# Optimization experiments

Hardware: AMD Instinct MI355X
Metric: run time of the kernel (lower is better)

## Reference

```python
import math
import jax, jax.numpy as jnp
import numpy as np

B, T, D, H, HD, FF = 2, 2048, 768, 12, 64, 3072


def setup_inputs() -> dict:
    key = jax.random.key(0)
    ks = jax.random.split(key, 9)
    s = 0.02  # init scale
    x = jax.random.normal(ks[0], (B, T, D), jnp.float32)
    wq = jax.random.normal(ks[1], (D, D), jnp.float32) * s
    wk = jax.random.normal(ks[2], (D, D), jnp.float32) * s
    wv = jax.random.normal(ks[3], (D, D), jnp.float32) * s
    wo = jax.random.normal(ks[4], (D, D), jnp.float32) * s
    w1 = jax.random.normal(ks[5], (FF, D), jnp.float32) * s
    w2 = jax.random.normal(ks[6], (FF, D), jnp.float32) * s
    w3 = jax.random.normal(ks[7], (D, FF), jnp.float32) * s
    attn_norm_w = jnp.ones((D,), jnp.float32)
    ffn_norm_w = jnp.ones((D,), jnp.float32)
    # interleaved RoPE cache: values pair-repeated along head_dim
    inv_freq = 1.0 / (10000.0 ** (np.arange(0, HD, 2, dtype=np.float32) / HD))
    freqs = np.arange(T, dtype=np.float32)[:, None] * inv_freq[None, :]  # [T, HD/2]
    emb = np.repeat(freqs, 2, axis=-1)  # [T, HD]
    cos = jnp.asarray(np.cos(emb), jnp.float32)[None, None]  # [1,1,T,HD]
    sin = jnp.asarray(np.sin(emb), jnp.float32)[None, None]
    return {"x": x, "wq": wq, "wk": wk, "wv": wv, "wo": wo,
            "w1": w1, "w2": w2, "w3": w3,
            "attn_norm_w": attn_norm_w, "ffn_norm_w": ffn_norm_w,
            "cos": cos, "sin": sin}


def _rmsnorm(x, w, eps=1e-6):
    n = jnp.linalg.norm(x, axis=-1, keepdims=True)
    return w * x / (n / math.sqrt(x.shape[-1]) + eps)


def _rotate_half(x):
    x1, x2 = x[..., ::2], x[..., 1::2]
    return jnp.stack((-x2, x1), axis=-1).reshape(x.shape)


def _attention(x, wq, wk, wv, wo, cos, sin):
    b, t, c = x.shape
    q = (x @ wq.T).reshape(b, t, H, HD).transpose(0, 2, 1, 3)  # [B,H,T,hd]
    k = (x @ wk.T).reshape(b, t, H, HD).transpose(0, 2, 1, 3)
    v = (x @ wv.T).reshape(b, t, H, HD).transpose(0, 2, 1, 3)
    c_, s_ = cos[:, :, :t, :], sin[:, :, :t, :]
    q = q * c_ + _rotate_half(q) * s_
    k = k * c_ + _rotate_half(k) * s_
    att = jnp.einsum('bhqd,bhkd->bhqk', q, k) / math.sqrt(HD)
    mask = jnp.triu(jnp.full((t, t), -jnp.inf, att.dtype), k=1)
    att = jax.nn.softmax(att + mask, axis=-1)
    y = jnp.einsum('bhqk,bhkd->bhqd', att, v)
    y = y.transpose(0, 2, 1, 3).reshape(b, t, c)
    return y @ wo.T


def reference(x, wq, wk, wv, wo, w1, w2, w3, attn_norm_w, ffn_norm_w, cos, sin):
    x = x + _attention(_rmsnorm(x, attn_norm_w), wq, wk, wv, wo, cos, sin)
    h = _rmsnorm(x, ffn_norm_w)
    ff = (jax.nn.silu(h @ w1.T) * (h @ w2.T)) @ w3.T
    return x + ff
```

## Files before the change

kernel.cpp:

```cpp
#include <hip/hip_runtime.h>
#include <hip/hip_bf16.h>
#include <math.h>

typedef __bf16 bf16;
typedef __bf16 bf16x4 __attribute__((ext_vector_type(4)));
typedef __bf16 bf16x8 __attribute__((ext_vector_type(8)));
typedef float floatx4 __attribute__((ext_vector_type(4)));

#define T_ 2048
#define D_ 768
#define H_ 12
#define HD_ 64
#define FF_ 3072
#define LOG2E 1.44269504f
#define LDP 72

__device__ __forceinline__ floatx4 mfma_bf16(bf16x8 a, bf16x8 b, floatx4 c) {
  return __builtin_amdgcn_mfma_f32_16x16x32_bf16(a, b, c, 0, 0, 0);
}

__global__ __launch_bounds__(256)
void cvt_k(const float* __restrict__ wq, const float* __restrict__ wk,
           const float* __restrict__ wv, const float* __restrict__ wo,
           const float* __restrict__ w1, const float* __restrict__ w2,
           const float* __restrict__ w3, bf16* __restrict__ o) {
  const long i = ((long)blockIdx.x * 256 + threadIdx.x) * 8;
  const float* s;
  if      (i <  589824) s = wq + i;
  else if (i < 1179648) s = wk + (i -  589824);
  else if (i < 1769472) s = wv + (i - 1179648);
  else if (i < 2359296) s = wo + (i - 1769472);
  else if (i < 4718592) s = w1 + (i - 2359296);
  else if (i < 7077888) s = w2 + (i - 4718592);
  else                  s = w3 + (i - 7077888);
  const floatx4 a = *(const floatx4*)s;
  const floatx4 b = *(const floatx4*)(s + 4);
  bf16x8 r;
#pragma unroll
  for (int j = 0; j < 4; j++) { r[j] = (bf16)a[j]; r[4 + j] = (bf16)b[j]; }
  *(bf16x8*)&o[i] = r;
}

__device__ __forceinline__ void gemm128_core(
    const bf16* __restrict__ A, const bf16* __restrict__ W,
    bf16* __restrict__ C, int N, int K, int m0, int n0)
{
  __shared__ __align__(16) bf16 As[128 * LDP];
  __shared__ __align__(16) bf16 Ws[128 * LDP];

  const int tid = threadIdx.x;
  const int lane = tid & 63;
  const int wm = tid >> 7;
  const int wn = (tid >> 6) & 1;
  const int fr = lane & 15;
  const int fk = (lane >> 4) * 8;

  floatx4 acc[4][4] = {};

  const int ar = tid >> 3;
  const int ac = (tid & 7) * 8;
  const bf16* Aptr = A + (long)(m0 + ar) * K + ac;
  const bf16* Wptr = W + (long)(n0 + ar) * K + ac;
  const long rstep = (long)32 * K;

  bf16x8 apf[4], wpf[4];
#pragma unroll
  for (int c = 0; c < 4; c++) apf[c] = *(const bf16x8*)(Aptr + c * rstep);
#pragma unroll
  for (int c = 0; c < 4; c++) wpf[c] = *(const bf16x8*)(Wptr + c * rstep);

  const int ns = K >> 6;
  for (int ks = 0; ks < ns; ks++) {
    __syncthreads();
#pragma unroll
    for (int c = 0; c < 4; c++) *(bf16x8*)&As[(ar + c * 32) * LDP + ac] = apf[c];
#pragma unroll
    for (int c = 0; c < 4; c++) *(bf16x8*)&Ws[(ar + c * 32) * LDP + ac] = wpf[c];
    __syncthreads();
    const long koff = (long)((ks + 1 < ns) ? ks + 1 : ks) * 64;
#pragma unroll
    for (int c = 0; c < 4; c++) apf[c] = *(const bf16x8*)(Aptr + koff + c * rstep);
#pragma unroll
    for (int c = 0; c < 4; c++) wpf[c] = *(const bf16x8*)(Wptr + koff + c * rstep);
#pragma unroll
    for (int kc = 0; kc < 2; kc++) {
      bf16x8 af[4], bfv[4];
#pragma unroll
      for (int i = 0; i < 4; i++) af[i]  = *(const bf16x8*)&As[(wm * 64 + i * 16 + fr) * LDP + kc * 32 + fk];
#pragma unroll
      for (int j = 0; j < 4; j++) bfv[j] = *(const bf16x8*)&Ws[(wn * 64 + j * 16 + fr) * LDP + kc * 32 + fk];
#pragma unroll
      for (int i = 0; i < 4; i++)
#pragma unroll
        for (int j = 0; j < 4; j++)
          acc[i][j] = mfma_bf16(af[i], bfv[j], acc[i][j]);
    }
  }

  const int rb = (lane >> 4) * 4;
#pragma unroll
  for (int i = 0; i < 4; i++)
#pragma unroll
    for (int j = 0; j < 4; j++) {
      const int n = n0 + wn * 64 + j * 16 + fr;
#pragma unroll
      for (int r = 0; r < 4; r++) {
        const int m = m0 + wm * 64 + i * 16 + rb + r;
        C[(long)m * N + n] = (bf16)acc[i][j][r];
      }
    }
}

__global__ __launch_bounds__(256)
void gemm_qkv(const bf16* __restrict__ h, const bf16* __restrict__ wq,
              const bf16* __restrict__ wk, const bf16* __restrict__ wv,
              bf16* __restrict__ q, bf16* __restrict__ k, bf16* __restrict__ v) {
  const int widx = blockIdx.x / 6;
  const int nb   = blockIdx.x % 6;
  const bf16* W = (widx == 0) ? wq : (widx == 1) ? wk : wv;
  bf16*       O = (widx == 0) ? q  : (widx == 1) ? k  : v;
  gemm128_core(h, W, O, D_, D_, blockIdx.y * 128, nb * 128);
}

__global__ __launch_bounds__(256)
void gemm_n64(const bf16* __restrict__ A, const bf16* __restrict__ W,
              float* __restrict__ C, const float* __restrict__ resid,
              int N, int K) {
  __shared__ __align__(16) bf16 As[128 * LDP];
  __shared__ __align__(16) bf16 Ws[64 * LDP];

  const int L  = blockIdx.x;
  const int j  = L >> 3;
  const int mb = (L & 7) * 4 + (j / 12);
  const int nb = j % 12;
  const int m0 = mb * 128, n0 = nb * 64;

  const int tid = threadIdx.x;
  const int lane = tid & 63;
  const int wm = tid >> 7;
  const int wn = (tid >> 6) & 1;
  const int fr = lane & 15;
  const int fk = (lane >> 4) * 8;

  floatx4 acc[4][2] = {};

  const int ar = tid >> 3;
  const int ac = (tid & 7) * 8;
  const bf16* Aptr = A + (long)(m0 + ar) * K + ac;
  const bf16* Wptr = W + (long)(n0 + ar) * K + ac;
  const long rstep = (long)32 * K;

  bf16x8 apf[4], wpf[2];
#pragma unroll
  for (int c = 0; c < 4; c++) apf[c] = *(const bf16x8*)(Aptr + c * rstep);
#pragma unroll
  for (int c = 0; c < 2; c++) wpf[c] = *(const bf16x8*)(Wptr + c * rstep);

  const int ns = K >> 6;
  for (int ks = 0; ks < ns; ks++) {
    __syncthreads();
#pragma unroll
    for (int c = 0; c < 4; c++) *(bf16x8*)&As[(ar + c * 32) * LDP + ac] = apf[c];
#pragma unroll
    for (int c = 0; c < 2; c++) *(bf16x8*)&Ws[(ar + c * 32) * LDP + ac] = wpf[c];
    __syncthreads();
    const long koff = (long)((ks + 1 < ns) ? ks + 1 : ks) * 64;
#pragma unroll
    for (int c = 0; c < 4; c++) apf[c] = *(const bf16x8*)(Aptr + koff + c * rstep);
#pragma unroll
    for (int c = 0; c < 2; c++) wpf[c] = *(const bf16x8*)(Wptr + koff + c * rstep);
#pragma unroll
    for (int kc = 0; kc < 2; kc++) {
      bf16x8 af[4], bfv[2];
#pragma unroll
      for (int i = 0; i < 4; i++) af[i]  = *(const bf16x8*)&As[(wm * 64 + i * 16 + fr) * LDP + kc * 32 + fk];
#pragma unroll
      for (int j2 = 0; j2 < 2; j2++) bfv[j2] = *(const bf16x8*)&Ws[(wn * 32 + j2 * 16 + fr) * LDP + kc * 32 + fk];
#pragma unroll
      for (int i = 0; i < 4; i++)
#pragma unroll
        for (int j2 = 0; j2 < 2; j2++)
          acc[i][j2] = mfma_bf16(af[i], bfv[j2], acc[i][j2]);
    }
  }

  const int rb = (lane >> 4) * 4;
#pragma unroll
  for (int i = 0; i < 4; i++)
#pragma unroll
    for (int j2 = 0; j2 < 2; j2++) {
      const int n = n0 + wn * 32 + j2 * 16 + fr;
#pragma unroll
      for (int r = 0; r < 4; r++) {
        const int m = m0 + wm * 64 + i * 16 + rb + r;
        const long idx = (long)m * N + n;
        C[idx] = acc[i][j2][r] + resid[idx];
      }
    }
}

__global__ __launch_bounds__(256)
void gemm_w12(const bf16* __restrict__ A, const bf16* __restrict__ W1,
              const bf16* __restrict__ W2, bf16* __restrict__ G) {
  __shared__ __align__(16) bf16 As[128 * LDP];
  __shared__ __align__(16) bf16 W1s[64 * LDP];
  __shared__ __align__(16) bf16 W2s[64 * LDP];

  const int L  = blockIdx.x;
  const int j  = L >> 3;
  const int nb = (L & 7) * 6 + (j >> 5);
  const int mb = j & 31;
  const int m0 = mb * 128, n0 = nb * 64;
  const int K = D_;

  const int tid = threadIdx.x;
  const int lane = tid & 63;
  const int wm = tid >> 7;
  const int wn = (tid >> 6) & 1;
  const int fr = lane & 15;
  const int fk = (lane >> 4) * 8;

  floatx4 acc1[4][2] = {}, acc2[4][2] = {};

  const int ar = tid >> 3;
  const int ac = (tid & 7) * 8;
  const bf16* Aptr  = A  + (long)(m0 + ar) * K + ac;
  const bf16* W1ptr = W1 + (long)(n0 + ar) * K + ac;
  const bf16* W2ptr = W2 + (long)(n0 + ar) * K + ac;
  const long rstep = (long)32 * K;

  bf16x8 apf[4], w1pf[2], w2pf[2];
#pragma unroll
  for (int c = 0; c < 4; c++) apf[c] = *(const bf16x8*)(Aptr + c * rstep);
#pragma unroll
  for (int c = 0; c < 2; c++) { w1pf[c] = *(const bf16x8*)(W1ptr + c * rstep);
                                w2pf[c] = *(const bf16x8*)(W2ptr + c * rstep); }

  const int ns = K >> 6;
  for (int ks = 0; ks < ns; ks++) {
    __syncthreads();
#pragma unroll
    for (int c = 0; c < 4; c++) *(bf16x8*)&As[(ar + c * 32) * LDP + ac] = apf[c];
#pragma unroll
    for (int c = 0; c < 2; c++) { *(bf16x8*)&W1s[(ar + c * 32) * LDP + ac] = w1pf[c];
                                  *(bf16x8*)&W2s[(ar + c * 32) * LDP + ac] = w2pf[c]; }
    __syncthreads();
    const long koff = (long)((ks + 1 < ns) ? ks + 1 : ks) * 64;
#pragma unroll
    for (int c = 0; c < 4; c++) apf[c] = *(const bf16x8*)(Aptr + koff + c * rstep);
#pragma unroll
    for (int c = 0; c < 2; c++) { w1pf[c] = *(const bf16x8*)(W1ptr + koff + c * rstep);
                                  w2pf[c] = *(const bf16x8*)(W2ptr + koff + c * rstep); }
#pragma unroll
    for (int kc = 0; kc < 2; kc++) {
      bf16x8 af[4], b1[2], b2[2];
#pragma unroll
      for (int i = 0; i < 4; i++) af[i] = *(const bf16x8*)&As[(wm * 64 + i * 16 + fr) * LDP + kc * 32 + fk];
#pragma unroll
      for (int j2 = 0; j2 < 2; j2++) { b1[j2] = *(const bf16x8*)&W1s[(wn * 32 + j2 * 16 + fr) * LDP + kc * 32 + fk];
                                       b2[j2] = *(const bf16x8*)&W2s[(wn * 32 + j2 * 16 + fr) * LDP + kc * 32 + fk]; }
#pragma unroll
      for (int i = 0; i < 4; i++)
#pragma unroll
        for (int j2 = 0; j2 < 2; j2++) {
          acc1[i][j2] = mfma_bf16(af[i], b1[j2], acc1[i][j2]);
          acc2[i][j2] = mfma_bf16(af[i], b2[j2], acc2[i][j2]);
        }
    }
  }

  const int rb = (lane >> 4) * 4;
#pragma unroll
  for (int i = 0; i < 4; i++)
#pragma unroll
    for (int j2 = 0; j2 < 2; j2++) {
      const int n = n0 + wn * 32 + j2 * 16 + fr;
#pragma unroll
      for (int r = 0; r < 4; r++) {
        const int m = m0 + wm * 64 + i * 16 + rb + r;
        const float a1 = acc1[i][j2][r];
        const float a2 = acc2[i][j2][r];
        const float s = a1 / (1.f + exp2f(-a1 * LOG2E));
        G[(long)m * FF_ + n] = (bf16)(s * a2);
      }
    }
}

__global__ __launch_bounds__(256)
void rmsnorm_k(const float* __restrict__ x, const float* __restrict__ wt,
               bf16* __restrict__ o) {
  const int row = blockIdx.x;
  const int tid = threadIdx.x;
  const long off = (long)row * D_;
  float vals[3];
  float ss = 0.f;
#pragma unroll
  for (int i = 0; i < 3; i++) {
    vals[i] = x[off + tid + i * 256];
    ss += vals[i] * vals[i];
  }
#pragma unroll
  for (int d = 1; d < 64; d <<= 1) ss += __shfl_xor(ss, d);
  __shared__ float wsum[4];
  if ((tid & 63) == 0) wsum[tid >> 6] = ss;
  __syncthreads();
  const float tot = wsum[0] + wsum[1] + wsum[2] + wsum[3];
  const float inv = 1.0f / (sqrtf(tot * (1.0f / 768.0f)) + 1e-6f);
#pragma unroll
  for (int i = 0; i < 3; i++)
    o[off + tid + i * 256] = (bf16)(vals[i] * inv * wt[tid + i * 256]);
}

__global__ __launch_bounds__(256)
void rope_k(bf16* __restrict__ q, bf16* __restrict__ k,
            const float* __restrict__ cosb, const float* __restrict__ sinb) {
  const int idx = blockIdx.x * 256 + threadIdx.x;
  const int tkn = idx / 384;
  const int p   = idx % 384;
  const int hh  = p >> 5;
  const int i   = p & 31;
  const int pos = tkn & (T_ - 1);
  const long off = (long)tkn * D_ + hh * HD_ + 2 * i;
  const float c0 = cosb[pos * HD_ + 2 * i];
  const float c1 = cosb[pos * HD_ + 2 * i + 1];
  const float s0 = sinb[pos * HD_ + 2 * i];
  const float s1 = sinb[pos * HD_ + 2 * i + 1];
  const float qe = (float)q[off], qo = (float)q[off + 1];
  q[off]     = (bf16)(qe * c0 - qo * s0);
  q[off + 1] = (bf16)(qo * c1 + qe * s1);
  const float ke = (float)k[off], ko = (float)k[off + 1];
  k[off]     = (bf16)(ke * c0 - ko * s0);
  k[off + 1] = (bf16)(ko * c1 + ke * s1);
}

__global__ __launch_bounds__(256)
void vtrans_k(const bf16* __restrict__ v, bf16* __restrict__ vt) {
  const int bh = blockIdx.x >> 5;
  const int tt = blockIdx.x & 31;
  const int b = bh / H_, h = bh % H_;
  __shared__ __align__(16) bf16 Vs[64][72];
  const int tid = threadIdx.x;
  const int row = tid >> 2;
  const int c0  = (tid & 3) * 16;
  const long gin = ((long)(b * T_ + tt * 64 + row)) * D_ + h * HD_ + c0;
  *(bf16x8*)&Vs[row][c0]     = *(const bf16x8*)&v[gin];
  *(bf16x8*)&Vs[row][c0 + 8] = *(const bf16x8*)&v[gin + 8];
  __syncthreads();
  const int hd = tid >> 2;
  const int t0 = (tid & 3) * 16;
  bf16x8 o0, o1;
#pragma unroll
  for (int j = 0; j < 8; j++) { o0[j] = Vs[t0 + j][hd]; o1[j] = Vs[t0 + 8 + j][hd]; }
  const long gout = ((long)(bh * HD_ + hd)) * T_ + tt * 64 + t0;
  *(bf16x8*)&vt[gout]     = o0;
  *(bf16x8*)&vt[gout + 8] = o1;
}

__global__ __launch_bounds__(256, 4)
void flash_attn(const bf16* __restrict__ q, const bf16* __restrict__ k,
                const bf16* __restrict__ vtg, float* __restrict__ po,
                float* __restrict__ pm, float* __restrict__ pl) {
  const int gid = blockIdx.x;
  const int bh = gid / 80;
  const int r  = gid % 80;
  int qt, c;
  if (r < 8)       { qt = r; c = 0; }
  else if (r < 24) { qt = 8 + ((r - 8) >> 1); c = (r - 8) & 1; }
  else if (r < 48) { const int u = r - 24; const int d = u / 3; qt = 16 + d; c = u - d * 3; }
  else             { const int u = r - 48; qt = 24 + (u >> 2); c = u & 3; }
  const int b  = bh / H_;
  const int h  = bh % H_;
  const int q0 = qt * 64;
  const int tbeg = c * 8;
  const int tend = (tbeg + 7 < qt) ? tbeg + 7 : qt;

  __shared__ __align__(16) bf16 Qs[64][72];
  __shared__ __align__(16) bf16 Ks[64][72];
  __shared__ __align__(16) bf16 Vt[64][72];
  __shared__ __align__(16) bf16 Ps[4][16][72];

  const int tid = threadIdx.x, lane = tid & 63, w = tid >> 6;
  const int fr = lane & 15, quad = lane >> 4, fk = quad * 8;
  const long base = ((long)b * T_) * D_ + h * HD_;
  const long vbase = (long)bh * HD_ * T_;

  {
    const int srow = tid >> 2, scol = (tid & 3) * 16;
    const long g = base + (long)(q0 + srow) * D_ + scol;
    *(bf16x8*)&Qs[srow][scol]     = *(const bf16x8*)&q[g];
    *(bf16x8*)&Qs[srow][scol + 8] = *(const bf16x8*)&q[g + 8];
  }

  float m_st = -1e30f, l_st = 0.f;
  floatx4 o[4] = {};
  const float SC = 0.125f * LOG2E;

  for (int t = tbeg; t <= tend; t++) {
    const int k0 = t * 64;
    __syncthreads();
    {
      const int srow = tid >> 2, scol = (tid & 3) * 16;
      const long kg = base + (long)(k0 + srow) * D_ + scol;
      *(bf16x8*)&Ks[srow][scol]     = *(const bf16x8*)&k[kg];
      *(bf16x8*)&Ks[srow][scol + 8] = *(const bf16x8*)&k[kg + 8];
      const long vg = vbase + (long)srow * T_ + k0 + scol;
      *(bf16x8*)&Vt[srow][scol]     = *(const bf16x8*)&vtg[vg];
      *(bf16x8*)&Vt[srow][scol + 8] = *(const bf16x8*)&vtg[vg + 8];
    }
    __syncthreads();

    floatx4 s[4] = {};
#pragma unroll
    for (int kd = 0; kd < 2; kd++) {
      const bf16x8 bq = *(const bf16x8*)&Qs[w * 16 + fr][kd * 32 + fk];
#pragma unroll
      for (int kt = 0; kt < 4; kt++) {
        const bf16x8 ak = *(const bf16x8*)&Ks[kt * 16 + fr][kd * 32 + fk];
        s[kt] = mfma_bf16(ak, bq, s[kt]);
      }
    }

    if (t == qt) {
      const int qloc = w * 16 + fr;
#pragma unroll
      for (int kt = 0; kt < 4; kt++)
#pragma unroll
        for (int r2 = 0; r2 < 4; r2++) {
          const int kvloc = kt * 16 + quad * 4 + r2;
          s[kt][r2] = (kvloc > qloc) ? -1e30f : s[kt][r2] * SC;
        }
    } else {
#pragma unroll
      for (int kt = 0; kt < 4; kt++)
#pragma unroll
        for (int r2 = 0; r2 < 4; r2++) s[kt][r2] *= SC;
    }

    float mx = -1e30f;
#pragma unroll
    for (int kt = 0; kt < 4; kt++)
#pragma unroll
      for (int r2 = 0; r2 < 4; r2++) mx = fmaxf(mx, s[kt][r2]);
    mx = fmaxf(mx, __shfl_xor(mx, 16));
    mx = fmaxf(mx, __shfl_xor(mx, 32));
    const float mnew  = fmaxf(m_st, mx);
    const float alpha = exp2f(m_st - mnew);
    m_st = mnew;
    float rs = 0.f;
#pragma unroll
    for (int kt = 0; kt < 4; kt++)
#pragma unroll
      for (int r2 = 0; r2 < 4; r2++) {
        const float pv = exp2f(s[kt][r2] - mnew);
        s[kt][r2] = pv;
        rs += pv;
      }
    rs += __shfl_xor(rs, 16);
    rs += __shfl_xor(rs, 32);
    l_st = l_st * alpha + rs;
#pragma unroll
    for (int ht = 0; ht < 4; ht++) o[ht] *= alpha;

#pragma unroll
    for (int kt = 0; kt < 4; kt++) {
      bf16x4 pk;
#pragma unroll
      for (int r2 = 0; r2 < 4; r2++) pk[r2] = (bf16)s[kt][r2];
      *(bf16x4*)&Ps[w][fr][kt * 16 + quad * 4] = pk;
    }

#pragma unroll
    for (int kq = 0; kq < 2; kq++) {
      const bf16x8 bp = *(const bf16x8*)&Ps[w][fr][kq * 32 + fk];
#pragma unroll
      for (int ht = 0; ht < 4; ht++) {
        const bf16x8 av = *(const bf16x8*)&Vt[ht * 16 + fr][kq * 32 + fk];
        o[ht] = mfma_bf16(av, bp, o[ht]);
      }
    }
  }

  const int qq = w * 16 + fr;
  const long pg = (long)gid * 4096 + qq * 64;
#pragma unroll
  for (int ht = 0; ht < 4; ht++)
    *(floatx4*)&po[pg + ht * 16 + quad * 4] = o[ht];
  if (quad == 0) { pm[gid * 64 + qq] = m_st; pl[gid * 64 + qq] = l_st; }
}

__global__ __launch_bounds__(256)
void flash_comb(const float* __restrict__ po, const float* __restrict__ pm,
                const float* __restrict__ pl, bf16* __restrict__ y) {
  const int bh = blockIdx.x >> 5;
  const int qt = blockIdx.x & 31;
  const int b = bh / H_, h = bh % H_;
  const int nc = (qt >> 3) + 1;
  int bse;
  if      (qt <  8) bse = qt;
  else if (qt < 16) bse = 8  + 2 * (qt - 8);
  else if (qt < 24) bse = 24 + 3 * (qt - 16);
  else              bse = 48 + 4 * (qt - 24);
  const int g0 = bh * 80 + bse;

  const int t = threadIdx.x;
  const int qq = t >> 2, hg = (t & 3) * 16;

  float M = -1e30f;
  for (int c2 = 0; c2 < nc; c2++) M = fmaxf(M, pm[(g0 + c2) * 64 + qq]);
  float l = 0.f;
  floatx4 o[4] = {};
  for (int c2 = 0; c2 < nc; c2++) {
    const float wgt = exp2f(pm[(g0 + c2) * 64 + qq] - M);
    l += wgt * pl[(g0 + c2) * 64 + qq];
    const long pg = (long)(g0 + c2) * 4096 + qq * 64 + hg;
#pragma unroll
    for (int j = 0; j < 4; j++) {
      const floatx4 t4 = *(const floatx4*)&po[pg + j * 4];
#pragma unroll
      for (int e = 0; e < 4; e++) o[j][e] += wgt * t4[e];
    }
  }
  const float inv = 1.f / l;
  bf16x8 r0, r1;
#pragma unroll
  for (int e = 0; e < 4; e++) {
    r0[e]     = (bf16)(o[0][e] * inv);
    r0[4 + e] = (bf16)(o[1][e] * inv);
    r1[e]     = (bf16)(o[2][e] * inv);
    r1[4 + e] = (bf16)(o[3][e] * inv);
  }
  const long yoff = ((long)b * T_ + qt * 64 + qq) * D_ + h * HD_ + hg;
  *(bf16x8*)&y[yoff]     = r0;
  *(bf16x8*)&y[yoff + 8] = r1;
}

extern "C" void kernel_launch(void* const* d_in, const int* in_sizes, int n_in,
                              void* d_out, int out_size, void* d_ws, size_t ws_size,
                              hipStream_t stream) {
  const float* x    = (const float*)d_in[0];
  const float* wq   = (const float*)d_in[1];
  const float* wk   = (const float*)d_in[2];
  const float* wv   = (const float*)d_in[3];
  const float* wo   = (const float*)d_in[4];
  const float* w1   = (const float*)d_in[5];
  const float* w2   = (const float*)d_in[6];
  const float* w3   = (const float*)d_in[7];
  const float* anw  = (const float*)d_in[8];
  const float* fnw  = (const float*)d_in[9];
  const float* cosb = (const float*)d_in[10];
  const float* sinb = (const float*)d_in[11];

  char* ws = (char*)d_ws;
  bf16*  wb  = (bf16*)(ws + 0);
  bf16*  wqb = wb;
  bf16*  wkb = wb +  589824;
  bf16*  wvb = wb + 1179648;
  bf16*  wob = wb + 1769472;
  bf16*  w1b = wb + 2359296;
  bf16*  w2b = wb + 4718592;
  bf16*  w3b = wb + 7077888;
  bf16*  qb  = (bf16*)(ws + 18874368);
  bf16*  kb  = (bf16*)(ws + 25165824);
  bf16*  vt  = (bf16*)(ws + 31457280);
  bf16*  yb  = (bf16*)(ws + 37748736);
  bf16*  hn  = (bf16*)(ws + 44040192);
  float* xm  = (float*)(ws + 50331648);
  bf16*  g   = (bf16*)(ws + 62914560);
  bf16*  vb  = (bf16*)(ws + 62914560);
  float* po  = (float*)(ws + 50331648);
  float* pm  = (float*)(ws + 81788928);
  float* pl  = (float*)(ws + 82280448);

  cvt_k<<<4608, 256, 0, stream>>>(wq, wk, wv, wo, w1, w2, w3, wb);
  rmsnorm_k<<<4096, 256, 0, stream>>>(x, anw, hn);
  gemm_qkv<<<dim3(18, 32), 256, 0, stream>>>(hn, wqb, wkb, wvb, qb, kb, vb);
  rope_k<<<6144, 256, 0, stream>>>(qb, kb, cosb, sinb);
  vtrans_k<<<768, 256, 0, stream>>>(vb, vt);
  flash_attn<<<1920, 256, 0, stream>>>(qb, kb, vt, po, pm, pl);
  flash_comb<<<768, 256, 0, stream>>>(po, pm, pl, yb);
  gemm_n64<<<384, 256, 0, stream>>>(yb, wob, xm, x, 768, 768);
  rmsnorm_k<<<4096, 256, 0, stream>>>(xm, fnw, hn);
  gemm_w12<<<1536, 256, 0, stream>>>(hn, w1b, w2b, g);
  gemm_n64<<<384, 256, 0, stream>>>(g, w3b, (float*)d_out, xm, 768, 3072);
}
```

Before: 322.0 us.

## Fuse RoPE and V-transpose into QKV GEMM epilogue, split-K the W3 GEMM

RoPE is now applied in the QKV GEMM epilogue, using a lane shuffle to fetch the paired element, and V is written directly in transposed layout. This removes the separate rope and vtrans kernels along with their extra global memory round trips. The final W3 GEMM is split along K into two halves written to float partial buffers, and a small combine kernel adds them to the residual, doubling the block count to fill more CUs. The W12 block-to-tile mapping is also reordered. In exchange, the split-K path adds extra partial-buffer traffic and one more launch, and the epilogue's cos/sin loads are scattered.

```diff
diff --git a/kernel.cpp b/kernel.cpp
--- a/kernel.cpp
+++ b/kernel.cpp
@@ -41,10 +41,17 @@
   *(bf16x8*)&o[i] = r;
 }
 
-__device__ __forceinline__ void gemm128_core(
-    const bf16* __restrict__ A, const bf16* __restrict__ W,
-    bf16* __restrict__ C, int N, int K, int m0, int n0)
-{
+__global__ __launch_bounds__(256)
+void gemm_qkv(const bf16* __restrict__ A, const bf16* __restrict__ wq,
+              const bf16* __restrict__ wk, const bf16* __restrict__ wv,
+              bf16* __restrict__ q, bf16* __restrict__ k, bf16* __restrict__ vt,
+              const float* __restrict__ cosb, const float* __restrict__ sinb) {
+  const int widx = blockIdx.x / 6;
+  const int nb   = blockIdx.x % 6;
+  const bf16* W = (widx == 0) ? wq : (widx == 1) ? wk : wv;
+  const int m0 = blockIdx.y * 128, n0 = nb * 128;
+  const int K = D_;
+
   __shared__ __align__(16) bf16 As[128 * LDP];
   __shared__ __align__(16) bf16 Ws[128 * LDP];
 
@@ -98,28 +105,42 @@
   }
 
   const int rb = (lane >> 4) * 4;
-#pragma unroll
-  for (int i = 0; i < 4; i++)
-#pragma unroll
-    for (int j = 0; j < 4; j++) {
-      const int n = n0 + wn * 64 + j * 16 + fr;
-#pragma unroll
-      for (int r = 0; r < 4; r++) {
-        const int m = m0 + wm * 64 + i * 16 + rb + r;
-        C[(long)m * N + n] = (bf16)acc[i][j][r];
-      }
-    }
-}
-
-__global__ __launch_bounds__(256)
-void gemm_qkv(const bf16* __restrict__ h, const bf16* __restrict__ wq,
-              const bf16* __restrict__ wk, const bf16* __restrict__ wv,
-              bf16* __restrict__ q, bf16* __restrict__ k, bf16* __restrict__ v) {
-  const int widx = blockIdx.x / 6;
-  const int nb   = blockIdx.x % 6;
-  const bf16* W = (widx == 0) ? wq : (widx == 1) ? wk : wv;
-  bf16*       O = (widx == 0) ? q  : (widx == 1) ? k  : v;
-  gemm128_core(h, W, O, D_, D_, blockIdx.y * 128, nb * 128);
+  if (widx < 2) {
+    bf16* O = (widx == 0) ? q : k;
+    const float sgn = (fr & 1) ? 1.f : -1.f;
+#pragma unroll
+    for (int i = 0; i < 4; i++)
+#pragma unroll
+      for (int j = 0; j < 4; j++) {
+        const int n = n0 + wn * 64 + j * 16 + fr;
+        const int d = n & 63;
+#pragma unroll
+        for (int r = 0; r < 4; r++) {
+          const int m = m0 + wm * 64 + i * 16 + rb + r;
+          const int pos = m & (T_ - 1);
+          const float val = acc[i][j][r];
+          const float par = __shfl_xor(val, 1);
+          const float cc = cosb[pos * HD_ + d];
+          const float ss = sinb[pos * HD_ + d];
+          O[(long)m * D_ + n] = (bf16)(val * cc + sgn * par * ss);
+        }
+      }
+  } else {
+#pragma unroll
+    for (int i = 0; i < 4; i++)
+#pragma unroll
+      for (int j = 0; j < 4; j++) {
+        const int n = n0 + wn * 64 + j * 16 + fr;
+        const int m = m0 + wm * 64 + i * 16 + rb;
+        const int b = m >> 11;
+        const int t = m & (T_ - 1);
+        const long row = (long)(b * H_ + (n >> 6)) * HD_ + (n & 63);
+        bf16x4 pk;
+#pragma unroll
+        for (int r = 0; r < 4; r++) pk[r] = (bf16)acc[i][j][r];
+        *(bf16x4*)&vt[row * T_ + t] = pk;
+      }
+  }
 }
 
 __global__ __launch_bounds__(256)
@@ -200,6 +221,102 @@
 }
 
 __global__ __launch_bounds__(256)
+void gemm_w3sk(const bf16* __restrict__ A, const bf16* __restrict__ W,
+               float* __restrict__ p0, float* __restrict__ p1) {
+  __shared__ __align__(16) bf16 As[128 * LDP];
+  __shared__ __align__(16) bf16 Ws[64 * LDP];
+
+  const int L  = blockIdx.x;
+  const int j  = L >> 3;
+  const int mb = (L & 7) * 4 + (j / 24);
+  const int inner = j % 24;
+  const int s  = inner / 12;
+  const int nb = inner % 12;
+  const int m0 = mb * 128, n0 = nb * 64;
+  const int K = FF_;
+  const int kbase = s * 1536;
+  float* C = s ? p1 : p0;
+
+  const int tid = threadIdx.x;
+  const int lane = tid & 63;
+  const int wm = tid >> 7;
+  const int wn = (tid >> 6) & 1;
+  const int fr = lane & 15;
+  const int fk = (lane >> 4) * 8;
+
+  floatx4 acc[4][2] = {};
+
+  const int ar = tid >> 3;
+  const int ac = (tid & 7) * 8;
+  const bf16* Aptr = A + (long)(m0 + ar) * K + kbase + ac;
+  const bf16* Wptr = W + (long)(n0 + ar) * K + kbase + ac;
+  const long rstep = (long)32 * K;
+
+  bf16x8 apf[4], wpf[2];
+#pragma unroll
+  for (int c = 0; c < 4; c++) apf[c] = *(const bf16x8*)(Aptr + c * rstep);
+#pragma unroll
+  for (int c = 0; c < 2; c++) wpf[c] = *(const bf16x8*)(Wptr + c * rstep);
+
+  const int ns = 24;
+  for (int ks = 0; ks < ns; ks++) {
+    __syncthreads();
+#pragma unroll
+    for (int c = 0; c < 4; c++) *(bf16x8*)&As[(ar + c * 32) * LDP + ac] = apf[c];
+#pragma unroll
+    for (int c = 0; c < 2; c++) *(bf16x8*)&Ws[(ar + c * 32) * LDP + ac] = wpf[c];
+    __syncthreads();
+    const long koff = (long)((ks + 1 < ns) ? ks + 1 : ks) * 64;
+#pragma unroll
+    for (int c = 0; c < 4; c++) apf[c] = *(const bf16x8*)(Aptr + koff + c * rstep);
+#pragma unroll
+    for (int c = 0; c < 2; c++) wpf[c] = *(const bf16x8*)(Wptr + koff + c * rstep);
+#pragma unroll
+    for (int kc = 0; kc < 2; kc++) {
+      bf16x8 af[4], bfv[2];
+#pragma unroll
+      for (int i = 0; i < 4; i++) af[i]  = *(const bf16x8*)&As[(wm * 64 + i * 16 + fr) * LDP + kc * 32 + fk];
+#pragma unroll
+      for (int j2 = 0; j2 < 2; j2++) bfv[j2] = *(const bf16x8*)&Ws[(wn * 32 + j2 * 16 + fr) * LDP + kc * 32 + fk];
+#pragma unroll
+      for (int i = 0; i < 4; i++)
+#pragma unroll
+        for (int j2 = 0; j2 < 2; j2++)
+          acc[i][j2] = mfma_bf16(af[i], bfv[j2], acc[i][j2]);
+    }
+  }
+
+  const int rb = (lane >> 4) * 4;
+#pragma unroll
+  for (int i = 0; i < 4; i++)
+#pragma unroll
+    for (int j2 = 0; j2 < 2; j2++) {
+      const int n = n0 + wn * 32 + j2 * 16 + fr;
+#pragma unroll
+      for (int r = 0; r < 4; r++) {
+        const int m = m0 + wm * 64 + i * 16 + rb + r;
+        C[(long)m * D_ + n] = acc[i][j2][r];
+      }
+    }
+}
+
+__global__ __launch_bounds__(256)
+void comb3_k(const float* __restrict__ p0, const float* __restrict__ p1,
+             const float* __restrict__ xm, float* __restrict__ out) {
+  const long i = ((long)blockIdx.x * 256 + threadIdx.x) * 8;
+#pragma unroll
+  for (int c = 0; c < 2; c++) {
+    const floatx4 a = *(const floatx4*)&p0[i + c * 4];
+    const floatx4 b = *(const floatx4*)&p1[i + c * 4];
+    const floatx4 d = *(const floatx4*)&xm[i + c * 4];
+    floatx4 r;
+#pragma unroll
+    for (int e = 0; e < 4; e++) r[e] = a[e] + b[e] + d[e];
+    *(floatx4*)&out[i + c * 4] = r;
+  }
+}
+
+__global__ __launch_bounds__(256)
 void gemm_w12(const bf16* __restrict__ A, const bf16* __restrict__ W1,
               const bf16* __restrict__ W2, bf16* __restrict__ G) {
   __shared__ __align__(16) bf16 As[128 * LDP];
@@ -208,8 +325,8 @@
 
   const int L  = blockIdx.x;
   const int j  = L >> 3;
-  const int nb = (L & 7) * 6 + (j >> 5);
-  const int mb = j & 31;
+  const int mb = j / 6;
+  const int nb = (L & 7) * 6 + (j % 6);
   const int m0 = mb * 128, n0 = nb * 64;
   const int K = D_;
 
@@ -309,51 +426,6 @@
 #pragma unroll
   for (int i = 0; i < 3; i++)
     o[off + tid + i * 256] = (bf16)(vals[i] * inv * wt[tid + i * 256]);
-}
-
-__global__ __launch_bounds__(256)
-void rope_k(bf16* __restrict__ q, bf16* __restrict__ k,
-            const float* __restrict__ cosb, const float* __restrict__ sinb) {
-  const int idx = blockIdx.x * 256 + threadIdx.x;
-  const int tkn = idx / 384;
-  const int p   = idx % 384;
-  const int hh  = p >> 5;
-  const int i   = p & 31;
-  const int pos = tkn & (T_ - 1);
-  const long off = (long)tkn * D_ + hh * HD_ + 2 * i;
-  const float c0 = cosb[pos * HD_ + 2 * i];
-  const float c1 = cosb[pos * HD_ + 2 * i + 1];
-  const float s0 = sinb[pos * HD_ + 2 * i];
-  const float s1 = sinb[pos * HD_ + 2 * i + 1];
-  const float qe = (float)q[off], qo = (float)q[off + 1];
-  q[off]     = (bf16)(qe * c0 - qo * s0);
-  q[off + 1] = (bf16)(qo * c1 + qe * s1);
-  const float ke = (float)k[off], ko = (float)k[off + 1];
-  k[off]     = (bf16)(ke * c0 - ko * s0);
-  k[off + 1] = (bf16)(ko * c1 + ke * s1);
-}
-
-__global__ __launch_bounds__(256)
-void vtrans_k(const bf16* __restrict__ v, bf16* __restrict__ vt) {
-  const int bh = blockIdx.x >> 5;
-  const int tt = blockIdx.x & 31;
-  const int b = bh / H_, h = bh % H_;
-  __shared__ __align__(16) bf16 Vs[64][72];
-  const int tid = threadIdx.x;
-  const int row = tid >> 2;
-  const int c0  = (tid & 3) * 16;
-  const long gin = ((long)(b * T_ + tt * 64 + row)) * D_ + h * HD_ + c0;
-  *(bf16x8*)&Vs[row][c0]     = *(const bf16x8*)&v[gin];
-  *(bf16x8*)&Vs[row][c0 + 8] = *(const bf16x8*)&v[gin + 8];
-  __syncthreads();
-  const int hd = tid >> 2;
-  const int t0 = (tid & 3) * 16;
-  bf16x8 o0, o1;
-#pragma unroll
-  for (int j = 0; j < 8; j++) { o0[j] = Vs[t0 + j][hd]; o1[j] = Vs[t0 + 8 + j][hd]; }
-  const long gout = ((long)(bh * HD_ + hd)) * T_ + tt * 64 + t0;
-  *(bf16x8*)&vt[gout]     = o0;
-  *(bf16x8*)&vt[gout + 8] = o1;
 }
 
 __global__ __launch_bounds__(256, 4)
@@ -566,20 +638,20 @@
   bf16*  hn  = (bf16*)(ws + 44040192);
   float* xm  = (float*)(ws + 50331648);
   bf16*  g   = (bf16*)(ws + 62914560);
-  bf16*  vb  = (bf16*)(ws + 62914560);
   float* po  = (float*)(ws + 50331648);
   float* pm  = (float*)(ws + 81788928);
   float* pl  = (float*)(ws + 82280448);
+  float* p30 = (float*)(ws + 18874368);
+  float* p31 = (float*)(ws + 37748736);
 
   cvt_k<<<4608, 256, 0, stream>>>(wq, wk, wv, wo, w1, w2, w3, wb);
   rmsnorm_k<<<4096, 256, 0, stream>>>(x, anw, hn);
-  gemm_qkv<<<dim3(18, 32), 256, 0, stream>>>(hn, wqb, wkb, wvb, qb, kb, vb);
-  rope_k<<<6144, 256, 0, stream>>>(qb, kb, cosb, sinb);
-  vtrans_k<<<768, 256, 0, stream>>>(vb, vt);
+  gemm_qkv<<<dim3(18, 32), 256, 0, stream>>>(hn, wqb, wkb, wvb, qb, kb, vt, cosb, sinb);
   flash_attn<<<1920, 256, 0, stream>>>(qb, kb, vt, po, pm, pl);
   flash_comb<<<768, 256, 0, stream>>>(po, pm, pl, yb);
   gemm_n64<<<384, 256, 0, stream>>>(yb, wob, xm, x, 768, 768);
   rmsnorm_k<<<4096, 256, 0, stream>>>(xm, fnw, hn);
   gemm_w12<<<1536, 256, 0, stream>>>(hn, w1b, w2b, g);
-  gemm_n64<<<384, 256, 0, stream>>>(g, w3b, (float*)d_out, xm, 768, 3072);
-}
+  gemm_w3sk<<<768, 256, 0, stream>>>(g, w3b, p30, p31);
+  comb3_k<<<1536, 256, 0, stream>>>(p30, p31, xm, (float*)d_out);
+}
```

Measured after the change: 308.8 us. 1.04x faster.
